# Optimization experiments

Hardware: AMD Instinct MI355X
Metric: run time of the kernel (lower is better)

## Reference

```python
import jax, jax.numpy as jnp
import numpy as np
from jax import lax

NE_RATIO = 0.8
SCALING_G = 1.0
W_FF = 30.0
SIG_EXT = 5.0
VT = 20.0
VR = 0.0
DT = 1e-3
NMAX = 60  # fixed Euler step count (Euler2fixedpt)
CONTRASTS = [0.0, 0.0432773, 0.103411, 0.186966, 0.303066, 0.464386, 0.68854, 1.0]
ORIENTS = [0., 15., 30., 45., 60., 75., 90., 105., 120., 135., 150., 165.]

# f_ricci polynomial coeffs in (-z), highest degree first (a9..a1, 0)
_FA = np.array([.14805913578876898, .64290613877355551, 1.0616084849547165,
                .93524391761244940, .62718906618071668, .32171431660633076,
                .32056016125642045, .77373949685442023, .22757881388024176, 0.0],
               dtype=np.float32)

def f_ricci(x):
    z = x / (1.0 + x)
    return jnp.log(2.0 * x + 1.0) + jnp.polyval(jnp.asarray(_FA), -z)

def g_ricci(x):
    z = x / (2.0 + x)
    num = z * (3.5441754117462949 + z * (-7.0529131065835378 + z * (-56.532378057580381
          + z * (279.56761105465944 + z * (-520.37554849441472 + z * (456.58245777026514
          + z * (-155.73340457809226)))))))
    den = 1.0 + z * (-4.1357968834226053 + z * (-7.2984226138266743 + z * (98.656602235468327
          + z * (-334.20436223415163 + z * (601.08633903294185 + z * (-599.58577549598340
          + z * (277.18420330693891 + z * (-16.445022798669722))))))))
    return num / den

def phi(mu, sigma, tau, tau_ref):
    """Ricciardi LIF transfer (Sanzeni rational approximation), branch-safe for jit."""
    xp = (mu - VR) / sigma
    xm = (mu - VT) / sigma
    cA = xm > 0
    cB = (xm <= 0) & (xp > 0)
    cC = xp <= 0
    xmA = jnp.where(cA, xm, 1.0); xpA = jnp.where(cA, xp, 2.0)
    rA = 1.0 / (f_ricci(xpA) - f_ricci(xmA))
    xmB = jnp.where(cB, xm, -1.0); xpB = jnp.where(cB, xp, 1.0)
    rB = 1.0 / (f_ricci(xpB) + jnp.exp(xmB * xmB) * g_ricci(-xmB))
    xmC = jnp.where(cC, xm, -2.0); xpC = jnp.where(cC, xp, -1.0)
    rC = jnp.exp(-xmC * xmC - jnp.log(g_ricci(-xmC) - jnp.exp(xpC * xpC - xmC * xmC) * g_ricci(-xpC)))
    r0 = jnp.where(cA, rA, jnp.where(cB, rB, rC))
    r0 = jnp.maximum(r0, 1e-30)
    return 1.0 / (tau_ref + tau / r0)

def _forward(hyperparameters, rand_mat, N):
    Ne = int(N * NE_RATIO); Ni = N - Ne
    pref = jnp.concatenate([
        jnp.linspace(0.0, 179.99, Ne, endpoint=False, dtype=jnp.float32),
        jnp.linspace(0.0, 179.99, Ni, endpoint=False, dtype=jnp.float32)])
    diff = jnp.abs(pref[:, None] - pref[None, :])              # [N,N]
    is_i = (jnp.arange(N) >= Ne).astype(jnp.int32)
    conn = is_i[:, None] + 2 * is_i[None, :]                   # 0:EE 1:IE 2:EI 3:II
    J = hyperparameters[0][conn]
    P = hyperparameters[1][conn]
    W = hyperparameters[2][conn]
    z = jnp.exp((jnp.cos(2.0 * jnp.pi / 180.0 * diff) - 1.0) / (4.0 * (jnp.pi / 180.0 * W) ** 2))
    weights = J * jax.nn.sigmoid(32.0 * (P * z - rand_mat))    # [N,N]
    weights2 = weights * weights
    tau = jnp.concatenate([0.01 * jnp.ones(Ne, jnp.float32), 0.01 * jnp.ones(Ni, jnp.float32)])
    T_inv = jnp.concatenate([100.0 * jnp.ones(Ne, jnp.float32), 200.0 * jnp.ones(Ni, jnp.float32)])
    tau_ref = jnp.concatenate([0.005 * jnp.ones(Ne, jnp.float32), 0.001 * jnp.ones(Ni, jnp.float32)])
    contrasts = jnp.asarray(CONTRASTS, jnp.float32)
    orients = jnp.asarray(ORIENTS, jnp.float32)
    dth = orients[None, :, None] - pref[None, None, :]         # [1,12,N]
    cg = jnp.exp((jnp.cos(2.0 * jnp.pi / 180.0 * dth) - 1.0) / (4.0 * (jnp.pi / 180.0 * W_FF) ** 2))
    mean = (contrasts[:, None, None] * 20.0 * SCALING_G * cg).reshape(-1, N)  # [96,N]
    sd2 = SIG_EXT * SIG_EXT

    def step(rate, _):
        mu = tau * (rate @ weights.T) + mean                   # [96,N]
        sig = jnp.sqrt(tau * (rate @ weights2.T) + sd2)
        rate = rate + DT * T_inv * (phi(mu, sig, tau, tau_ref) - rate)
        return rate, None

    rate, _ = lax.scan(step, jnp.zeros_like(mean), None, length=NMAX)
    all_rates = rate.reshape(len(CONTRASTS), len(ORIENTS), N)
    return jnp.transpose(all_rates, (2, 0, 1))                 # [N, 8, 12]

def setup_inputs():
    key = jax.random.key(0)
    hyperparameters = jnp.array([[1.99, 1.9, -1.01, -0.79],
                                 [0.11, 0.11, 0.45, 0.45],
                                 [32.0, 32.0, 32.0, 32.0]], dtype=jnp.float32)
    rand_mat = jax.random.uniform(key, (1500, 1500), dtype=jnp.float32)
    return {"hyperparameters": hyperparameters, "rand_mat": rand_mat, "neuron_num": 1500}

def reference(hyperparameters, rand_mat, neuron_num):
    return _forward(hyperparameters, rand_mat, neuron_num)
```

## Files before the change

kernel.cpp:

```cpp
#include <hip/hip_runtime.h>
#include <hip/hip_bf16.h>
#include <math.h>

#define NN      1500
#define NEE     1200
#define NPAD    1536
#define BATCH   96
#define NSTEP   60
#define PI_F    3.14159265358979323846f

#define NWG     192
#define GRPWG   96
#define SUBWG   12
#define NTHR    1024
#define WAVES   16
#define KSLW    (NPAD / WAVES)
#define BH      48
#define MFR     3

#define BP      49
#define SLOTF   (2 * 16 * BP)
#define LDS_BYTES (WAVES * SLOTF * 4)

typedef __attribute__((ext_vector_type(8))) short short8b;
typedef __attribute__((ext_vector_type(4))) float f32x4;


__device__ __forceinline__ ushort bf16_rn(float x) {
    unsigned u = __float_as_uint(x);
    unsigned r = (u + 0x7FFFu + ((u >> 16) & 1u)) >> 16;
    return (ushort)r;
}
__device__ __forceinline__ float bf16f(ushort h) {
    return __uint_as_float(((unsigned)h) << 16);
}

__device__ __forceinline__ short8b load16_sc1(const ushort* p) {
    short8b r;
    asm volatile("global_load_dwordx4 %0, %1, off sc0 sc1"
                 : "=v"(r) : "v"((unsigned long long)(uintptr_t)p));
    return r;
}


__device__ __forceinline__ float f_ricci(float x) {
    float z = x / (1.0f + x);
    float t = -z;
    float p = 0.14805913578876898f;
    p = p * t + 0.64290613877355551f;
    p = p * t + 1.0616084849547165f;
    p = p * t + 0.93524391761244940f;
    p = p * t + 0.62718906618071668f;
    p = p * t + 0.32171431660633076f;
    p = p * t + 0.32056016125642045f;
    p = p * t + 0.77373949685442023f;
    p = p * t + 0.22757881388024176f;
    p = p * t;
    return logf(2.0f * x + 1.0f) + p;
}

__device__ __forceinline__ float g_ricci(float x) {
    float z = x / (2.0f + x);
    float num = z * (3.5441754117462949f + z * (-7.0529131065835378f + z * (-56.532378057580381f
        + z * (279.56761105465944f + z * (-520.37554849441472f + z * (456.58245777026514f
        + z * (-155.73340457809226f)))))));
    float den = 1.0f + z * (-4.1357968834226053f + z * (-7.2984226138266743f + z * (98.656602235468327f
        + z * (-334.20436223415163f + z * (601.08633903294185f + z * (-599.58577549598340f
        + z * (277.18420330693891f + z * (-16.445022798669722f))))))));
    return num / den;
}

__device__ __forceinline__ float phi_lif(float mu, float sig, float tau, float tau_ref) {
    float xp = mu / sig;
    float xm = (mu - 20.0f) / sig;
    float r0;
    if (xm > 0.0f) {
        r0 = 1.0f / (f_ricci(xp) - f_ricci(xm));
    } else if (xp > 0.0f) {
        r0 = 1.0f / (f_ricci(xp) + expf(xm * xm) * g_ricci(-xm));
    } else {
        float a = g_ricci(-xm) - expf(xp * xp - xm * xm) * g_ricci(-xp);
        r0 = expf(-xm * xm - logf(a));
    }
    r0 = fmaxf(r0, 1e-30f);
    return 1.0f / (tau_ref + tau / r0);
}

__device__ __forceinline__ float pref_of(int n) {
    const float stepE = 179.99f / 1200.0f;
    const float stepI = 179.99f / 300.0f;
    return (n < NEE) ? (float)n * stepE : (float)(n - NEE) * stepI;
}


__global__ __launch_bounds__(256) void k_weights(const float* __restrict__ hyp,
        const float* __restrict__ rand_mat,
        ushort* __restrict__ Whi, ushort* __restrict__ Wlo,
        ushort* __restrict__ W2hi, ushort* __restrict__ W2lo) {
    int k = blockIdx.x * 256 + threadIdx.x;
    int i = blockIdx.y;
    size_t idx = (size_t)i * NPAD + k;
    if (i >= NN || k >= NN) {
        Whi[idx] = 0; Wlo[idx] = 0; W2hi[idx] = 0; W2lo[idx] = 0;
        return;
    }
    float diff = fabsf(pref_of(i) - pref_of(k));
    int conn = (i >= NEE ? 1 : 0) + 2 * (k >= NEE ? 1 : 0);
    float J  = hyp[conn];
    float P  = hyp[4 + conn];
    float Wp = hyp[8 + conn];
    float dn = 4.0f * (PI_F / 180.0f * Wp) * (PI_F / 180.0f * Wp);
    float z = expf((cosf(2.0f * PI_F / 180.0f * diff) - 1.0f) / dn);
    float x = 32.0f * (P * z - rand_mat[(size_t)i * NN + k]);
    float w = J / (1.0f + expf(-x));
    float w2 = w * w;
    ushort h = bf16_rn(w);
    Whi[idx] = h;  Wlo[idx] = bf16_rn(w - bf16f(h));
    ushort h2 = bf16_rn(w2);
    W2hi[idx] = h2; W2lo[idx] = bf16_rn(w2 - bf16f(h2));
}


__global__ __launch_bounds__(256) void k_init(ushort* __restrict__ rhiA,
                                              ushort* __restrict__ rloA,
                                              uint* __restrict__ cnt) {
    int i = blockIdx.x * 256 + threadIdx.x;
    int b = blockIdx.y;
    size_t idx = (size_t)b * NPAD + i;
    rhiA[idx] = 0;
    rloA[idx] = 0;
    if (blockIdx.x == 0 && blockIdx.y == 0) {
        for (int t = threadIdx.x; t < 1024; t += 256) cnt[t] = 0;
    }
}


__global__ __launch_bounds__(NTHR) void k_coop(
        const ushort* __restrict__ Whi, const ushort* __restrict__ Wlo,
        const ushort* __restrict__ W2hi, const ushort* __restrict__ W2lo,
        ushort* __restrict__ rhiA, ushort* __restrict__ rloA,
        ushort* __restrict__ rhiB, ushort* __restrict__ rloB,
        uint* __restrict__ cnt, float* __restrict__ out)
{
    extern __shared__ float sm[];
    const int tid  = threadIdx.x;
    const int wave = tid >> 6;
    const int lane = tid & 63;
    const int lr   = lane & 15;
    const int lq   = lane >> 4;
    const int bx   = blockIdx.x;
    const int it   = bx % 96;
    const int bhf  = bx / 96;
    const int i0   = it * 16;
    const int b0   = bhf * BH;
    const int kb   = wave * KSLW;

    const int c  = tid & 15;
    const int bb = tid >> 4;
    const int ig = i0 + c;
    const int gb = b0 + bb;
    const size_t gx = (size_t)gb * NPAD + ig;
    const bool upd = (tid < BH * 16);

    const float contrasts[8] = {0.0f, 0.0432773f, 0.103411f, 0.186966f,
                                0.303066f, 0.464386f, 0.68854f, 1.0f};
    const float dnff = 4.0f * (PI_F / 180.0f * 30.0f) * (PI_F / 180.0f * 30.0f);
    float mean0 = 0.0f;
    if (upd && ig < NN) {
        float dth = 15.0f * (float)(gb % 12) - pref_of(ig);
        mean0 = contrasts[gb / 12] * 20.0f *
                expf((cosf(2.0f * PI_F / 180.0f * dth) - 1.0f) / dnff);
    }
    float rr = 0.0f;

    const size_t bof = (size_t)(i0 + lr) * NPAD + kb + lq * 8;
    size_t aofm[MFR];
#pragma unroll
    for (int m = 0; m < MFR; m++)
        aofm[m] = (size_t)(b0 + m * 16 + lr) * NPAD + kb + lq * 8;

    for (int s = 0; s < NSTEP; s++) {
        const ushort* rin_hi = (s & 1) ? rhiB : rhiA;
        const ushort* rin_lo = (s & 1) ? rloB : rloA;
        ushort* rout_hi = (s & 1) ? rhiA : rhiB;
        ushort* rout_lo = (s & 1) ? rloA : rloB;

        f32x4 acc1[MFR], acc2[MFR];
#pragma unroll
        for (int m = 0; m < MFR; m++) {
            acc1[m] = (f32x4){0.0f, 0.0f, 0.0f, 0.0f};
            acc2[m] = (f32x4){0.0f, 0.0f, 0.0f, 0.0f};
        }

#pragma unroll
        for (int kk = 0; kk < KSLW / 32; kk++) {
            const int ko = kk * 32;
            short8b wh  = *(const short8b*)(Whi  + bof + ko);
            short8b wl  = *(const short8b*)(Wlo  + bof + ko);
            short8b w2h = *(const short8b*)(W2hi + bof + ko);
            short8b w2l = *(const short8b*)(W2lo + bof + ko);
            short8b ah[MFR], al[MFR];
#pragma unroll
            for (int m = 0; m < MFR; m++) {
                ah[m] = load16_sc1(rin_hi + aofm[m] + ko);
                al[m] = load16_sc1(rin_lo + aofm[m] + ko);
            }
            asm volatile("s_waitcnt vmcnt(0)" ::: "memory");
            __builtin_amdgcn_sched_barrier(0);
#pragma unroll
            for (int m = 0; m < MFR; m++) {
                acc1[m] = __builtin_amdgcn_mfma_f32_16x16x32_bf16(ah[m], wh,  acc1[m], 0, 0, 0);
                acc1[m] = __builtin_amdgcn_mfma_f32_16x16x32_bf16(ah[m], wl,  acc1[m], 0, 0, 0);
                acc1[m] = __builtin_amdgcn_mfma_f32_16x16x32_bf16(al[m], wh,  acc1[m], 0, 0, 0);
                acc2[m] = __builtin_amdgcn_mfma_f32_16x16x32_bf16(ah[m], w2h, acc2[m], 0, 0, 0);
                acc2[m] = __builtin_amdgcn_mfma_f32_16x16x32_bf16(ah[m], w2l, acc2[m], 0, 0, 0);
                acc2[m] = __builtin_amdgcn_mfma_f32_16x16x32_bf16(al[m], w2h, acc2[m], 0, 0, 0);
            }
        }

        {
            float* sp = sm + wave * SLOTF;
#pragma unroll
            for (int m = 0; m < MFR; m++) {
                float* p1 = sp + lr * BP + m * 16 + 4 * lq;
                float* p2 = p1 + 16 * BP;
                *(f32x4*)p1 = acc1[m];
                *(f32x4*)p2 = acc2[m];
            }
        }
        __syncthreads();

        if (upd) {
            float rn = 0.0f;
            if (ig < NN) {
                float u1 = 0.0f, u2 = 0.0f;
#pragma unroll
                for (int w = 0; w < WAVES; w++) {
                    u1 += sm[w * SLOTF + c * BP + bb];
                    u2 += sm[w * SLOTF + (16 + c) * BP + bb];
                }
                float mu = 0.01f * u1 + mean0;
                float sg = sqrtf(0.01f * u2 + 25.0f);
                float tr = (ig < NEE) ? 0.005f : 0.001f;
                float Ti = (ig < NEE) ? 100.0f : 200.0f;
                float ph = phi_lif(mu, sg, 0.01f, tr);
                rr = rr + 1e-3f * Ti * (ph - rr);
                rn = rr;
                if (s == NSTEP - 1) out[(size_t)ig * BATCH + gb] = rn;
            }
            int hh = (int)bf16_rn(rn);
            int ll = (int)bf16_rn(rn - bf16f((ushort)hh));
            int hN = __shfl_down(hh, 1);
            int lN = __shfl_down(ll, 1);
            if ((c & 1) == 0) {
                uint hp = (uint)hh | ((uint)hN << 16);
                uint lp = (uint)ll | ((uint)lN << 16);
                __hip_atomic_store((uint*)(rout_hi + gx), hp,
                                   __ATOMIC_RELAXED, __HIP_MEMORY_SCOPE_AGENT);
                __hip_atomic_store((uint*)(rout_lo + gx), lp,
                                   __ATOMIC_RELAXED, __HIP_MEMORY_SCOPE_AGENT);
            }
        }

        __syncthreads();
        if (tid == 0) {
            const int g = bx & 7;
            uint* sub = cnt + (size_t)(bhf * 8 + g) * 32;
            uint* mst = cnt + (size_t)(16 + bhf) * 32;
            uint* flg = cnt + (size_t)(18 + bhf) * 32;
            const uint sv = (uint)(s + 1);
            uint old = __hip_atomic_fetch_add(sub, 1u,
                           __ATOMIC_RELAXED, __HIP_MEMORY_SCOPE_AGENT);
            if (old == sv * SUBWG - 1u) {
                uint mo = __hip_atomic_fetch_add(mst, 1u,
                              __ATOMIC_RELAXED, __HIP_MEMORY_SCOPE_AGENT);
                if (mo == sv * 8u - 1u) {
                    __hip_atomic_store(flg, sv,
                        __ATOMIC_RELAXED, __HIP_MEMORY_SCOPE_AGENT);
                } else {
                    while (__hip_atomic_load(flg, __ATOMIC_RELAXED,
                               __HIP_MEMORY_SCOPE_AGENT) < sv)
                        __builtin_amdgcn_s_sleep(1);
                }
            } else {
                while (__hip_atomic_load(flg, __ATOMIC_RELAXED,
                           __HIP_MEMORY_SCOPE_AGENT) < sv)
                    __builtin_amdgcn_s_sleep(1);
            }
        }
        __syncthreads();
    }
}


extern "C" void kernel_launch(void* const* d_in, const int* in_sizes, int n_in,
                              void* d_out, int out_size, void* d_ws, size_t ws_size,
                              hipStream_t stream) {
    const float* hyp      = (const float*)d_in[0];
    const float* rand_mat = (const float*)d_in[1];
    float* out            = (float*)d_out;

    char* p = (char*)d_ws;
    ushort* Whi  = (ushort*)p; p += (size_t)NPAD * NPAD * 2;
    ushort* Wlo  = (ushort*)p; p += (size_t)NPAD * NPAD * 2;
    ushort* W2hi = (ushort*)p; p += (size_t)NPAD * NPAD * 2;
    ushort* W2lo = (ushort*)p; p += (size_t)NPAD * NPAD * 2;
    ushort* rhiA = (ushort*)p; p += (size_t)BATCH * NPAD * 2;
    ushort* rloA = (ushort*)p; p += (size_t)BATCH * NPAD * 2;
    ushort* rhiB = (ushort*)p; p += (size_t)BATCH * NPAD * 2;
    ushort* rloB = (ushort*)p; p += (size_t)BATCH * NPAD * 2;
    uint*   cnt  = (uint*)p;   p += 4096;

    hipFuncSetAttribute((const void*)k_coop,
                        hipFuncAttributeMaxDynamicSharedMemorySize, LDS_BYTES);

    k_weights<<<dim3(NPAD / 256, NPAD), 256, 0, stream>>>(hyp, rand_mat,
                                                          Whi, Wlo, W2hi, W2lo);
    k_init<<<dim3(NPAD / 256, BATCH), 256, 0, stream>>>(rhiA, rloA, cnt);

    void* args[] = {(void*)&Whi, (void*)&Wlo, (void*)&W2hi, (void*)&W2lo,
                    (void*)&rhiA, (void*)&rloA, (void*)&rhiB, (void*)&rloB,
                    (void*)&cnt, (void*)&out};
    hipLaunchCooperativeKernel((const void*)k_coop, dim3(NWG), dim3(NTHR),
                               args, LDS_BYTES, stream);
}
```

Before: 1.003 ms.

## Retile workgroups to 48 neurons x 16 batch rows with 32-WG sync groups

Result: slower. 1.614 ms (+61.0%).

```diff
diff --git a/kernel.cpp b/kernel.cpp
--- a/kernel.cpp
+++ b/kernel.cpp
@@ -10,16 +10,16 @@
 #define PI_F    3.14159265358979323846f
 
 #define NWG     192
-#define GRPWG   96
-#define SUBWG   12
+#define GRPWG   32
 #define NTHR    1024
 #define WAVES   16
 #define KSLW    (NPAD / WAVES)
-#define BH      48
+#define IW      48
+#define BW_     16
 #define MFR     3
 
-#define BP      49
-#define SLOTF   (2 * 16 * BP)
+#define BPI     52
+#define SLOTF   (2 * BW_ * BPI)
 #define LDS_BYTES (WAVES * SLOTF * 4)
 
 typedef __attribute__((ext_vector_type(8))) short short8b;
@@ -149,18 +149,18 @@
     const int lr   = lane & 15;
     const int lq   = lane >> 4;
     const int bx   = blockIdx.x;
-    const int it   = bx % 96;
-    const int bhf  = bx / 96;
-    const int i0   = it * 16;
-    const int b0   = bhf * BH;
+    const int it   = (bx & 7) * 4 + ((bx >> 3) & 3);
+    const int bg   = bx >> 5;
+    const int i0   = it * IW;
+    const int b0   = bg * BW_;
     const int kb   = wave * KSLW;
 
-    const int c  = tid & 15;
-    const int bb = tid >> 4;
+    const int c  = tid % IW;
+    const int bb = tid / IW;
     const int ig = i0 + c;
     const int gb = b0 + bb;
     const size_t gx = (size_t)gb * NPAD + ig;
-    const bool upd = (tid < BH * 16);
+    const bool upd = (tid < IW * BW_);
 
     const float contrasts[8] = {0.0f, 0.0432773f, 0.103411f, 0.186966f,
                                 0.303066f, 0.464386f, 0.68854f, 1.0f};
@@ -173,11 +173,11 @@
     }
     float rr = 0.0f;
 
-    const size_t bof = (size_t)(i0 + lr) * NPAD + kb + lq * 8;
-    size_t aofm[MFR];
-#pragma unroll
-    for (int m = 0; m < MFR; m++)
-        aofm[m] = (size_t)(b0 + m * 16 + lr) * NPAD + kb + lq * 8;
+    size_t wof[MFR];
+#pragma unroll
+    for (int f = 0; f < MFR; f++)
+        wof[f] = (size_t)(i0 + f * 16 + lr) * NPAD + kb + lq * 8;
+    const size_t aof = (size_t)(b0 + lr) * NPAD + kb + lq * 8;
 
     for (int s = 0; s < NSTEP; s++) {
         const ushort* rin_hi = (s & 1) ? rhiB : rhiA;
@@ -187,45 +187,45 @@
 
         f32x4 acc1[MFR], acc2[MFR];
 #pragma unroll
-        for (int m = 0; m < MFR; m++) {
-            acc1[m] = (f32x4){0.0f, 0.0f, 0.0f, 0.0f};
-            acc2[m] = (f32x4){0.0f, 0.0f, 0.0f, 0.0f};
+        for (int f = 0; f < MFR; f++) {
+            acc1[f] = (f32x4){0.0f, 0.0f, 0.0f, 0.0f};
+            acc2[f] = (f32x4){0.0f, 0.0f, 0.0f, 0.0f};
         }
 
 #pragma unroll
         for (int kk = 0; kk < KSLW / 32; kk++) {
             const int ko = kk * 32;
-            short8b wh  = *(const short8b*)(Whi  + bof + ko);
-            short8b wl  = *(const short8b*)(Wlo  + bof + ko);
-            short8b w2h = *(const short8b*)(W2hi + bof + ko);
-            short8b w2l = *(const short8b*)(W2lo + bof + ko);
-            short8b ah[MFR], al[MFR];
-#pragma unroll
-            for (int m = 0; m < MFR; m++) {
-                ah[m] = load16_sc1(rin_hi + aofm[m] + ko);
-                al[m] = load16_sc1(rin_lo + aofm[m] + ko);
-            }
+            short8b wh[MFR], wl[MFR], w2h[MFR], w2l[MFR];
+#pragma unroll
+            for (int f = 0; f < MFR; f++) {
+                wh[f]  = *(const short8b*)(Whi  + wof[f] + ko);
+                wl[f]  = *(const short8b*)(Wlo  + wof[f] + ko);
+                w2h[f] = *(const short8b*)(W2hi + wof[f] + ko);
+                w2l[f] = *(const short8b*)(W2lo + wof[f] + ko);
+            }
+            short8b ah = load16_sc1(rin_hi + aof + ko);
+            short8b al = load16_sc1(rin_lo + aof + ko);
             asm volatile("s_waitcnt vmcnt(0)" ::: "memory");
             __builtin_amdgcn_sched_barrier(0);
 #pragma unroll
-            for (int m = 0; m < MFR; m++) {
-                acc1[m] = __builtin_amdgcn_mfma_f32_16x16x32_bf16(ah[m], wh,  acc1[m], 0, 0, 0);
-                acc1[m] = __builtin_amdgcn_mfma_f32_16x16x32_bf16(ah[m], wl,  acc1[m], 0, 0, 0);
-                acc1[m] = __builtin_amdgcn_mfma_f32_16x16x32_bf16(al[m], wh,  acc1[m], 0, 0, 0);
-                acc2[m] = __builtin_amdgcn_mfma_f32_16x16x32_bf16(ah[m], w2h, acc2[m], 0, 0, 0);
-                acc2[m] = __builtin_amdgcn_mfma_f32_16x16x32_bf16(ah[m], w2l, acc2[m], 0, 0, 0);
-                acc2[m] = __builtin_amdgcn_mfma_f32_16x16x32_bf16(al[m], w2h, acc2[m], 0, 0, 0);
+            for (int f = 0; f < MFR; f++) {
+                acc1[f] = __builtin_amdgcn_mfma_f32_16x16x32_bf16(wh[f],  ah, acc1[f], 0, 0, 0);
+                acc1[f] = __builtin_amdgcn_mfma_f32_16x16x32_bf16(wl[f],  ah, acc1[f], 0, 0, 0);
+                acc1[f] = __builtin_amdgcn_mfma_f32_16x16x32_bf16(wh[f],  al, acc1[f], 0, 0, 0);
+                acc2[f] = __builtin_amdgcn_mfma_f32_16x16x32_bf16(w2h[f], ah, acc2[f], 0, 0, 0);
+                acc2[f] = __builtin_amdgcn_mfma_f32_16x16x32_bf16(w2l[f], ah, acc2[f], 0, 0, 0);
+                acc2[f] = __builtin_amdgcn_mfma_f32_16x16x32_bf16(w2h[f], al, acc2[f], 0, 0, 0);
             }
         }
 
         {
             float* sp = sm + wave * SLOTF;
 #pragma unroll
-            for (int m = 0; m < MFR; m++) {
-                float* p1 = sp + lr * BP + m * 16 + 4 * lq;
-                float* p2 = p1 + 16 * BP;
-                *(f32x4*)p1 = acc1[m];
-                *(f32x4*)p2 = acc2[m];
+            for (int f = 0; f < MFR; f++) {
+                float* p1 = sp + lr * BPI + f * 16 + 4 * lq;
+                float* p2 = p1 + BW_ * BPI;
+                *(f32x4*)p1 = acc1[f];
+                *(f32x4*)p2 = acc2[f];
             }
         }
         __syncthreads();
@@ -236,8 +236,8 @@
                 float u1 = 0.0f, u2 = 0.0f;
 #pragma unroll
                 for (int w = 0; w < WAVES; w++) {
-                    u1 += sm[w * SLOTF + c * BP + bb];
-                    u2 += sm[w * SLOTF + (16 + c) * BP + bb];
+                    u1 += sm[w * SLOTF + bb * BPI + c];
+                    u2 += sm[w * SLOTF + BW_ * BPI + bb * BPI + c];
                 }
                 float mu = 0.01f * u1 + mean0;
                 float sg = sqrtf(0.01f * u2 + 25.0f);
@@ -264,24 +264,14 @@
 
         __syncthreads();
         if (tid == 0) {
-            const int g = bx & 7;
-            uint* sub = cnt + (size_t)(bhf * 8 + g) * 32;
-            uint* mst = cnt + (size_t)(16 + bhf) * 32;
-            uint* flg = cnt + (size_t)(18 + bhf) * 32;
+            uint* ctr = cnt + (size_t)bg * 64;
+            uint* flg = cnt + 512 + (size_t)bg * 64;
             const uint sv = (uint)(s + 1);
-            uint old = __hip_atomic_fetch_add(sub, 1u,
+            uint old = __hip_atomic_fetch_add(ctr, 1u,
                            __ATOMIC_RELAXED, __HIP_MEMORY_SCOPE_AGENT);
-            if (old == sv * SUBWG - 1u) {
-                uint mo = __hip_atomic_fetch_add(mst, 1u,
-                              __ATOMIC_RELAXED, __HIP_MEMORY_SCOPE_AGENT);
-                if (mo == sv * 8u - 1u) {
-                    __hip_atomic_store(flg, sv,
-                        __ATOMIC_RELAXED, __HIP_MEMORY_SCOPE_AGENT);
-                } else {
-                    while (__hip_atomic_load(flg, __ATOMIC_RELAXED,
-                               __HIP_MEMORY_SCOPE_AGENT) < sv)
-                        __builtin_amdgcn_s_sleep(1);
-                }
+            if (old == sv * GRPWG - 1u) {
+                __hip_atomic_store(flg, sv,
+                    __ATOMIC_RELAXED, __HIP_MEMORY_SCOPE_AGENT);
             } else {
                 while (__hip_atomic_load(flg, __ATOMIC_RELAXED,
                            __HIP_MEMORY_SCOPE_AGENT) < sv)
```
